# Performance work log

Hardware: AMD Instinct MI355X
Metric: run time of the kernel (lower is better)

Reference implementation:

```python
import jax, jax.numpy as jnp
import numpy as np

IMAGES_PER_GPU = 2
IMAGE_MAX_DIM = 1024.0
POOL_SIZE = 7
NUM_ROIS = 1000


def crop_and_resize_level(fm0, boxes, pool_size):
    """TF-style crop_and_resize (bilinear, extrapolation_value=0).
    fm0: [C,H,W] feature map of image 0 (box_indices are all zero in the source).
    boxes: [N,4] normalized (y1,x1,y2,x2).
    returns crops: [N,C,pool_size,pool_size]
    """
    C, H, W = fm0.shape
    P = pool_size
    y1, x1, y2, x2 = boxes[:, 0], boxes[:, 1], boxes[:, 2], boxes[:, 3]
    t = jnp.arange(P, dtype=fm0.dtype) / (P - 1)  # [P]
    # sample coords in source pixel space: [N,P]
    ys = (y1[:, None] + t[None, :] * (y2 - y1)[:, None]) * (H - 1)
    xs = (x1[:, None] + t[None, :] * (x2 - x1)[:, None]) * (W - 1)
    valid_y = (ys >= 0) & (ys <= H - 1)
    valid_x = (xs >= 0) & (xs <= W - 1)
    ysc = jnp.clip(ys, 0.0, H - 1)
    xsc = jnp.clip(xs, 0.0, W - 1)
    y0 = jnp.floor(ysc).astype(jnp.int32)
    x0 = jnp.floor(xsc).astype(jnp.int32)
    y1i = jnp.minimum(y0 + 1, H - 1)
    x1i = jnp.minimum(x0 + 1, W - 1)
    ly = (ysc - y0)  # [N,P]
    lx = (xsc - x0)  # [N,P]

    def g(yi, xi):
        # advanced indexing broadcast -> [C,N,P,P]
        return fm0[:, yi[:, :, None], xi[:, None, :]]

    tl = g(y0, x0)
    tr = g(y0, x1i)
    bl = g(y1i, x0)
    br = g(y1i, x1i)
    lx_b = lx[None, :, None, :]
    ly_b = ly[None, :, :, None]
    top = tl + (tr - tl) * lx_b
    bot = bl + (br - bl) * lx_b
    out = top + (bot - top) * ly_b  # [C,N,P,P]
    mask = (valid_y[:, :, None] & valid_x[:, None, :])  # [N,P,P]
    out = out * mask[None].astype(out.dtype)
    return jnp.transpose(out, (1, 0, 2, 3))  # [N,C,P,P]


def roi_align(feature_maps, rois_flat, pool_size):
    """feature_maps: list of 4 arrays [B,256,Hl,Wl] for levels 2..5.
    rois_flat: [N,4] pixel coords (x1,y1,x2,y2). Returns [N,256,P,P]."""
    x1, y1, x2, y2 = rois_flat[:, 0], rois_flat[:, 1], rois_flat[:, 2], rois_flat[:, 3]
    area = (y2 - y1) * (x2 - x1)
    roi_level = jnp.log2(jnp.sqrt(jnp.maximum(area, 0.0)) / 224.0)
    roi_level = jnp.clip(jnp.round(roi_level) + 4, 2, 5)
    # boxes normalized and reordered (x1,y1,x2,y2) -> (y1,x1,y2,x2)
    boxes = rois_flat[:, jnp.array([1, 0, 3, 2])] / IMAGE_MAX_DIM
    N = rois_flat.shape[0]
    C = feature_maps[0].shape[1]
    pooled = jnp.zeros((N, C, pool_size, pool_size), dtype=feature_maps[0].dtype)
    for i, level in enumerate(range(2, 6)):
        crops = crop_and_resize_level(feature_maps[i][0], boxes, pool_size)
        sel = (roi_level == level)[:, None, None, None]
        pooled = jnp.where(sel, crops, pooled)
    return pooled


def setup_inputs() -> dict:
    key = jax.random.key(0)
    k2, k3, k4, k5, kxy, kwh = jax.random.split(key, 6)
    B, R = IMAGES_PER_GPU, NUM_ROIS
    p2 = jax.random.normal(k2, (B, 256, 256, 256), dtype=jnp.float32)
    p3 = jax.random.normal(k3, (B, 256, 128, 128), dtype=jnp.float32)
    p4 = jax.random.normal(k4, (B, 256, 64, 64), dtype=jnp.float32)
    p5 = jax.random.normal(k5, (B, 256, 32, 32), dtype=jnp.float32)
    xy1 = jax.random.uniform(kxy, (B, R, 2), minval=0.0, maxval=1000.0)
    wh = jax.random.uniform(kwh, (B, R, 2), minval=8.0, maxval=512.0)
    xy2 = jnp.clip(xy1 + wh, 0.0, IMAGE_MAX_DIM)
    rois = jnp.concatenate([xy1, xy2], axis=-1).astype(jnp.float32)  # (x1,y1,x2,y2)
    return {"p2": p2, "p3": p3, "p4": p4, "p5": p5, "rois": rois}


def reference(p2, p3, p4, p5, rois):
    B, R = rois.shape[0], rois.shape[1]
    rois_flat = rois.reshape(B * R, 4)
    pooled = roi_align([p2, p3, p4, p5], rois_flat, POOL_SIZE)
    return pooled.reshape(B, R, 256, POOL_SIZE, POOL_SIZE)
```

## Files before the change

kernel.cpp:

```cpp
#include <hip/hip_runtime.h>

#define P 7
#define PP 49
#define CMAX 256
#define ACTIVE 245

typedef float f2 __attribute__((ext_vector_type(2), aligned(4)));

struct PixParam { int o00, o10; float w00, w01, w10, w11; };

__global__ __launch_bounds__(256) void roialign_kernel(
    const float* __restrict__ p2, const float* __restrict__ p3,
    const float* __restrict__ p4, const float* __restrict__ p5,
    const float* __restrict__ rois, float* __restrict__ out)
{
    __shared__ PixParam sp[PP];

    const int r = blockIdx.x;
    const int t = threadIdx.x;

    const float x1 = rois[r * 4 + 0];
    const float y1 = rois[r * 4 + 1];
    const float x2 = rois[r * 4 + 2];
    const float y2 = rois[r * 4 + 3];

    const float area = __fmul_rn(__fsub_rn(y2, y1), __fsub_rn(x2, x1));
    int lvl = (int)rintf(log2f(sqrtf(fmaxf(area, 0.0f)) / 224.0f)) + 4;
    lvl = lvl < 2 ? 2 : (lvl > 5 ? 5 : lvl);
    const int H = 1024 >> lvl;
    const int HW = H * H;
    const float* fm = (lvl == 2) ? p2 : (lvl == 3) ? p3 : (lvl == 4) ? p4 : p5;

    if (t < PP) {
        const int py = t / P, px = t % P;
        const float inv = 1.0f / 1024.0f;
        const float by1 = __fmul_rn(y1, inv), bx1 = __fmul_rn(x1, inv);
        const float by2 = __fmul_rn(y2, inv), bx2 = __fmul_rn(x2, inv);
        const float Hm1 = (float)(H - 1);
        const float ty = (float)py / 6.0f;
        const float tx = (float)px / 6.0f;
        const float vy = __fmul_rn(__fadd_rn(by1, __fmul_rn(ty, __fsub_rn(by2, by1))), Hm1);
        const float vx = __fmul_rn(__fadd_rn(bx1, __fmul_rn(tx, __fsub_rn(bx2, bx1))), Hm1);
        const bool vldy = (vy >= 0.0f) && (vy <= Hm1);
        const bool vldx = (vx >= 0.0f) && (vx <= Hm1);
        const float yc = fminf(fmaxf(vy, 0.0f), Hm1);
        const float xc = fminf(fmaxf(vx, 0.0f), Hm1);
        const int y0 = (int)floorf(yc);
        const int x0 = (int)floorf(xc);
        const int y1i = min(y0 + 1, H - 1);
        const float ly = __fsub_rn(yc, (float)y0);
        const float lx = __fsub_rn(xc, (float)x0);
        const float m = (vldy && vldx) ? 1.0f : 0.0f;
        const float wy0 = m * (1.0f - ly), wy1 = m * ly;
        const float wx0 = 1.0f - lx,      wx1 = lx;
        PixParam pp;
        pp.o00 = y0 * H + x0;
        pp.o10 = y1i * H + x0;
        pp.w00 = wy0 * wx0;     pp.w01 = wy0 * wx1;
        pp.w10 = wy1 * wx0;     pp.w11 = wy1 * wx1;
        sp[t] = pp;
    }
    __syncthreads();

    if (t >= ACTIVE) return;
    const int pix = t % PP;
    const int c0  = t / PP;
    const PixParam pp = sp[pix];

    const float* fmc = fm + (size_t)c0 * HW;
    float* outr = out + (size_t)r * (CMAX * PP);
    int idx = t;
    #pragma unroll 8
    for (int c = c0; c < CMAX; c += 5) {
        const f2 tp = *(const f2*)(fmc + pp.o00);
        const f2 bt = *(const f2*)(fmc + pp.o10);
        outr[idx] = tp.x * pp.w00 + tp.y * pp.w01 + bt.x * pp.w10 + bt.y * pp.w11;
        fmc += 5 * HW;
        idx += ACTIVE;
    }
}

extern "C" void kernel_launch(void* const* d_in, const int* in_sizes, int n_in,
                              void* d_out, int out_size, void* d_ws, size_t ws_size,
                              hipStream_t stream) {
    const float* p2   = (const float*)d_in[0];
    const float* p3   = (const float*)d_in[1];
    const float* p4   = (const float*)d_in[2];
    const float* p5   = (const float*)d_in[3];
    const float* rois = (const float*)d_in[4];
    float* out = (float*)d_out;
    const int n_rois = in_sizes[4] / 4;
    roialign_kernel<<<n_rois, 256, 0, stream>>>(p2, p3, p4, p5, rois, out);
}
```

Measured before the change: 339.6 us.

## Sort ROIs by level and spatial bin, process clustered groups per block

Adds a counting-sort pre-pass (zero, histogram, scan, scatter kernels) that orders ROIs by pyramid level and coarse 8x8 spatial bin. The main kernel then handles 8 spatially adjacent ROIs per block over a 32-channel slice, with 8-way independent loads per thread. The aim is better cache reuse of overlapping feature-map regions and more memory-level parallelism. In exchange it adds four small kernel launches, atomics, and workspace traffic, and output writes become scattered across ROIs.

Measured after the change: 300.3 us. -11.6%, faster.

```diff
diff --git a/kernel.cpp b/kernel.cpp
--- a/kernel.cpp
+++ b/kernel.cpp
@@ -3,80 +3,171 @@
 #define P 7
 #define PP 49
 #define CMAX 256
-#define ACTIVE 245
+#define G 8
+#define CSPLIT 8
+#define CSLICE 32
+#define NBINS 256
+
+#define WS_HIST   0
+#define WS_CURSOR 256
+#define WS_BUCKET 512
+#define WS_PERM   2560
 
 typedef float f2 __attribute__((ext_vector_type(2), aligned(4)));
 
 struct PixParam { int o00, o10; float w00, w01, w10, w11; };
 
-__global__ __launch_bounds__(256) void roialign_kernel(
+__device__ __forceinline__ int roi_level(float x1, float y1, float x2, float y2) {
+    const float area = __fmul_rn(__fsub_rn(y2, y1), __fsub_rn(x2, x1));
+    int lvl = (int)rintf(log2f(sqrtf(fmaxf(area, 0.0f)) / 224.0f)) + 4;
+    return lvl < 2 ? 2 : (lvl > 5 ? 5 : lvl);
+}
+
+__global__ void zero_kernel(unsigned* ws) {
+    ws[WS_HIST + threadIdx.x] = 0u;
+}
+
+__global__ void hist_kernel(const float* __restrict__ rois, int n, unsigned* ws) {
+    const int r = blockIdx.x * blockDim.x + threadIdx.x;
+    if (r >= n) return;
+    const float x1 = rois[r*4+0], y1 = rois[r*4+1], x2 = rois[r*4+2], y2 = rois[r*4+3];
+    const int lvl = roi_level(x1, y1, x2, y2);
+    int cx = ((int)(__fmul_rn(__fadd_rn(x1, x2), 0.5f))) >> 7; cx = min(cx, 7);
+    int cy = ((int)(__fmul_rn(__fadd_rn(y1, y2), 0.5f))) >> 7; cy = min(cy, 7);
+    const int b = ((lvl - 2) << 6) | (cy << 3) | cx;
+    ws[WS_BUCKET + r] = (unsigned)b;
+    atomicAdd(&ws[WS_HIST + b], 1u);
+}
+
+__global__ void scan_kernel(unsigned* ws) {
+    __shared__ unsigned s[NBINS];
+    const int t = threadIdx.x;
+    const unsigned h = ws[WS_HIST + t];
+    s[t] = h;
+    __syncthreads();
+    for (int off = 1; off < NBINS; off <<= 1) {
+        const unsigned v = (t >= off) ? s[t - off] : 0u;
+        __syncthreads();
+        s[t] += v;
+        __syncthreads();
+    }
+    ws[WS_CURSOR + t] = s[t] - h;
+}
+
+__global__ void scatter_kernel(int n, unsigned* ws) {
+    const int r = blockIdx.x * blockDim.x + threadIdx.x;
+    if (r >= n) return;
+    const unsigned b = ws[WS_BUCKET + r];
+    const unsigned pos = atomicAdd(&ws[WS_CURSOR + b], 1u);
+    ws[WS_PERM + pos] = (unsigned)r;
+}
+
+__global__ __launch_bounds__(256) void roialign_main(
     const float* __restrict__ p2, const float* __restrict__ p3,
     const float* __restrict__ p4, const float* __restrict__ p5,
-    const float* __restrict__ rois, float* __restrict__ out)
+    const float* __restrict__ rois, const unsigned* __restrict__ ws,
+    float* __restrict__ out, int n)
 {
-    __shared__ PixParam sp[PP];
+    __shared__ PixParam sp[G * PP];
+    __shared__ const float* fm_s[G];
+    __shared__ int hw_s[G];
+    __shared__ long long obase_s[G];
 
-    const int r = blockIdx.x;
-    const int t = threadIdx.x;
+    const int nclust = (n + G - 1) / G;
+    const int cl = blockIdx.x % nclust;
+    const int cb = blockIdx.x / nclust;
+    const int t  = threadIdx.x;
 
-    const float x1 = rois[r * 4 + 0];
-    const float y1 = rois[r * 4 + 1];
-    const float x2 = rois[r * 4 + 2];
-    const float y2 = rois[r * 4 + 3];
+    for (int idx = t; idx < G * PP; idx += 256) {
+        const int g = idx / PP, pix = idx % PP;
+        const int gi = cl * G + g;
+        PixParam pp; pp.o00 = 0; pp.o10 = 0;
+        pp.w00 = 0.f; pp.w01 = 0.f; pp.w10 = 0.f; pp.w11 = 0.f;
+        if (gi < n) {
+            const int rr = (int)ws[WS_PERM + gi];
+            const float x1 = rois[rr*4+0], y1 = rois[rr*4+1];
+            const float x2 = rois[rr*4+2], y2 = rois[rr*4+3];
+            const int lvl = roi_level(x1, y1, x2, y2);
+            const int H = 1024 >> lvl;
+            const float* fm = (lvl == 2) ? p2 : (lvl == 3) ? p3 : (lvl == 4) ? p4 : p5;
 
-    const float area = __fmul_rn(__fsub_rn(y2, y1), __fsub_rn(x2, x1));
-    int lvl = (int)rintf(log2f(sqrtf(fmaxf(area, 0.0f)) / 224.0f)) + 4;
-    lvl = lvl < 2 ? 2 : (lvl > 5 ? 5 : lvl);
-    const int H = 1024 >> lvl;
-    const int HW = H * H;
-    const float* fm = (lvl == 2) ? p2 : (lvl == 3) ? p3 : (lvl == 4) ? p4 : p5;
-
-    if (t < PP) {
-        const int py = t / P, px = t % P;
-        const float inv = 1.0f / 1024.0f;
-        const float by1 = __fmul_rn(y1, inv), bx1 = __fmul_rn(x1, inv);
-        const float by2 = __fmul_rn(y2, inv), bx2 = __fmul_rn(x2, inv);
-        const float Hm1 = (float)(H - 1);
-        const float ty = (float)py / 6.0f;
-        const float tx = (float)px / 6.0f;
-        const float vy = __fmul_rn(__fadd_rn(by1, __fmul_rn(ty, __fsub_rn(by2, by1))), Hm1);
-        const float vx = __fmul_rn(__fadd_rn(bx1, __fmul_rn(tx, __fsub_rn(bx2, bx1))), Hm1);
-        const bool vldy = (vy >= 0.0f) && (vy <= Hm1);
-        const bool vldx = (vx >= 0.0f) && (vx <= Hm1);
-        const float yc = fminf(fmaxf(vy, 0.0f), Hm1);
-        const float xc = fminf(fmaxf(vx, 0.0f), Hm1);
-        const int y0 = (int)floorf(yc);
-        const int x0 = (int)floorf(xc);
-        const int y1i = min(y0 + 1, H - 1);
-        const float ly = __fsub_rn(yc, (float)y0);
-        const float lx = __fsub_rn(xc, (float)x0);
-        const float m = (vldy && vldx) ? 1.0f : 0.0f;
-        const float wy0 = m * (1.0f - ly), wy1 = m * ly;
-        const float wx0 = 1.0f - lx,      wx1 = lx;
-        PixParam pp;
-        pp.o00 = y0 * H + x0;
-        pp.o10 = y1i * H + x0;
-        pp.w00 = wy0 * wx0;     pp.w01 = wy0 * wx1;
-        pp.w10 = wy1 * wx0;     pp.w11 = wy1 * wx1;
-        sp[t] = pp;
+            const int py = pix / P, px = pix % P;
+            const float inv = 1.0f / 1024.0f;
+            const float by1 = __fmul_rn(y1, inv), bx1 = __fmul_rn(x1, inv);
+            const float by2 = __fmul_rn(y2, inv), bx2 = __fmul_rn(x2, inv);
+            const float Hm1 = (float)(H - 1);
+            const float ty = (float)py / 6.0f;
+            const float tx = (float)px / 6.0f;
+            const float vy = __fmul_rn(__fadd_rn(by1, __fmul_rn(ty, __fsub_rn(by2, by1))), Hm1);
+            const float vx = __fmul_rn(__fadd_rn(bx1, __fmul_rn(tx, __fsub_rn(bx2, bx1))), Hm1);
+            const bool vldy = (vy >= 0.0f) && (vy <= Hm1);
+            const bool vldx = (vx >= 0.0f) && (vx <= Hm1);
+            const float yc = fminf(fmaxf(vy, 0.0f), Hm1);
+            const float xc = fminf(fmaxf(vx, 0.0f), Hm1);
+            const int y0 = (int)floorf(yc);
+            const int x0 = (int)floorf(xc);
+            const int y1i = min(y0 + 1, H - 1);
+            const float ly = __fsub_rn(yc, (float)y0);
+            const float lx = __fsub_rn(xc, (float)x0);
+            const float m = (vldy && vldx) ? 1.0f : 0.0f;
+            const float wy0 = m * (1.0f - ly), wy1 = m * ly;
+            const float wx0 = 1.0f - lx,      wx1 = lx;
+            pp.o00 = y0 * H + x0;
+            pp.o10 = y1i * H + x0;
+            pp.w00 = wy0 * wx0;  pp.w01 = wy0 * wx1;
+            pp.w10 = wy1 * wx0;  pp.w11 = wy1 * wx1;
+            if (pix == 0) {
+                fm_s[g] = fm;
+                hw_s[g] = H * H;
+                obase_s[g] = (long long)rr * (CMAX * PP);
+            }
+        } else if (pix == 0) {
+            fm_s[g] = p2; hw_s[g] = 0; obase_s[g] = -1;
+        }
+        sp[idx] = pp;
     }
     __syncthreads();
 
-    if (t >= ACTIVE) return;
+    if (t >= 5 * PP) return;
     const int pix = t % PP;
     const int c0  = t / PP;
-    const PixParam pp = sp[pix];
 
-    const float* fmc = fm + (size_t)c0 * HW;
-    float* outr = out + (size_t)r * (CMAX * PP);
-    int idx = t;
-    #pragma unroll 8
-    for (int c = c0; c < CMAX; c += 5) {
-        const f2 tp = *(const f2*)(fmc + pp.o00);
-        const f2 bt = *(const f2*)(fmc + pp.o10);
-        outr[idx] = tp.x * pp.w00 + tp.y * pp.w01 + bt.x * pp.w10 + bt.y * pp.w11;
-        fmc += 5 * HW;
-        idx += ACTIVE;
+    const float* pT[G]; const float* pB[G];
+    size_t step[G];
+    float w00[G], w01[G], w10[G], w11[G];
+    long long ob[G];
+    #pragma unroll
+    for (int g = 0; g < G; ++g) {
+        const PixParam pp = sp[g * PP + pix];
+        const int hw = hw_s[g];
+        const float* base = fm_s[g] + (size_t)(cb * CSLICE + c0) * hw;
+        pT[g] = base + pp.o00;
+        pB[g] = base + pp.o10;
+        step[g] = (size_t)5 * hw;
+        w00[g] = pp.w00; w01[g] = pp.w01; w10[g] = pp.w10; w11[g] = pp.w11;
+        ob[g] = obase_s[g];
+    }
+
+    #pragma unroll
+    for (int k = 0; k < 7; ++k) {
+        const int clc = c0 + 5 * k;
+        if (clc < CSLICE) {
+            f2 tp[G], bt[G];
+            #pragma unroll
+            for (int g = 0; g < G; ++g) {
+                tp[g] = *(const f2*)pT[g];
+                bt[g] = *(const f2*)pB[g];
+                pT[g] += step[g]; pB[g] += step[g];
+            }
+            #pragma unroll
+            for (int g = 0; g < G; ++g) {
+                const float v = tp[g].x * w00[g] + tp[g].y * w01[g]
+                              + bt[g].x * w10[g] + bt[g].y * w11[g];
+                if (ob[g] >= 0) {
+                    out[ob[g] + (long long)(cb * CSLICE + clc) * PP + pix] = v;
+                }
+            }
+        }
     }
 }
 
@@ -89,6 +180,15 @@
     const float* p5   = (const float*)d_in[3];
     const float* rois = (const float*)d_in[4];
     float* out = (float*)d_out;
-    const int n_rois = in_sizes[4] / 4;
-    roialign_kernel<<<n_rois, 256, 0, stream>>>(p2, p3, p4, p5, rois, out);
+    unsigned* ws = (unsigned*)d_ws;
+    const int n = in_sizes[4] / 4;
+
+    const int nb = (n + 255) / 256;
+    zero_kernel<<<1, NBINS, 0, stream>>>(ws);
+    hist_kernel<<<nb, 256, 0, stream>>>(rois, n, ws);
+    scan_kernel<<<1, NBINS, 0, stream>>>(ws);
+    scatter_kernel<<<nb, 256, 0, stream>>>(n, ws);
+
+    const int nclust = (n + G - 1) / G;
+    roialign_main<<<nclust * CSPLIT, 256, 0, stream>>>(p2, p3, p4, p5, rois, ws, out, n);
 }
```
